# Performance work log

Measured on AMD Instinct MI355X. Metric: run time of the kernel, lower is better.

## Reference

```python
import jax, jax.numpy as jnp
import numpy as np

B, L, H, NH, NB = 16, 200, 128, 2, 2
ITEMS, SPAN = 50000, 256
NEG = -2.0**32 + 1.0  # mask value used by the torch module


def _ln(x, g, b, eps=1e-8):
    m = jnp.mean(x, axis=-1, keepdims=True)
    v = jnp.mean((x - m) ** 2, axis=-1, keepdims=True)
    return (x - m) / jnp.sqrt(v + eps) * g + b


def setup_inputs() -> dict:
    key = jax.random.key(0)
    ks = jax.random.split(key, 20)
    p = lambda k, s: (jax.random.normal(k, s, jnp.float32) * 0.02)
    item_emb = p(ks[0], (ITEMS + 1, H)).at[0].set(0.0)  # padding_idx=0
    return {
        "user_ids": jax.random.randint(ks[1], (B,), 0, 10000),
        "log_seqs": jax.random.randint(ks[2], (B, L), 0, ITEMS),
        "time_matrices": jax.random.randint(ks[3], (B, L, L), 0, SPAN),
        "pos_seqs": jax.random.randint(ks[4], (B, L), 0, ITEMS),
        "neg_seqs": jax.random.randint(ks[5], (B, L), 0, ITEMS),
        "item_emb": item_emb,
        "pos_K_emb": p(ks[6], (L, H)),
        "pos_V_emb": p(ks[7], (L, H)),
        "time_K_emb": p(ks[8], (SPAN + 1, H)),
        "time_V_emb": p(ks[9], (SPAN + 1, H)),
        "Wq": p(ks[10], (NB, H, H)), "bq": jnp.zeros((NB, H)),
        "Wk": p(ks[11], (NB, H, H)), "bk": jnp.zeros((NB, H)),
        "Wv": p(ks[12], (NB, H, H)), "bv": jnp.zeros((NB, H)),
        "ln1_g": jnp.ones((NB, H)), "ln1_b": jnp.zeros((NB, H)),
        "W1": p(ks[13], (NB, H, H)), "b1": jnp.zeros((NB, H)),
        "W2": p(ks[14], (NB, H, H)), "b2": jnp.zeros((NB, H)),
        "ln2_g": jnp.ones((NB, H)), "ln2_b": jnp.zeros((NB, H)),
        "lnf_g": jnp.ones((H,)), "lnf_b": jnp.zeros((H,)),
    }


def reference(user_ids, log_seqs, time_matrices, pos_seqs, neg_seqs,
              item_emb, pos_K_emb, pos_V_emb, time_K_emb, time_V_emb,
              Wq, bq, Wk, bk, Wv, bv, ln1_g, ln1_b,
              W1, b1, W2, b2, ln2_g, ln2_b, lnf_g, lnf_b):
    d = H // NH
    pad = (log_seqs == 0)                    # (B,L) timeline mask
    keep = (~pad)[..., None].astype(jnp.float32)

    seqs = item_emb[log_seqs] * jnp.sqrt(jnp.float32(H))
    seqs = seqs * keep
    posK = pos_K_emb.reshape(L, NH, d)       # same for every batch element
    posV = pos_V_emb.reshape(L, NH, d)
    tmK = time_K_emb[time_matrices].reshape(B, L, L, NH, d)  # (B,L,L,h,d)
    tmV = time_V_emb[time_matrices].reshape(B, L, L, NH, d)
    causal = ~jnp.tril(jnp.ones((L, L), dtype=bool))          # True = masked
    mask = pad[:, None, :, None] | causal[None, None, :, :]   # (B,1,L,L) row-mask | causal

    for i in range(NB):
        Q = (seqs @ Wq[i].T + bq[i]).reshape(B, L, NH, d)
        K = (seqs @ Wk[i].T + bk[i]).reshape(B, L, NH, d)
        V = (seqs @ Wv[i].T + bv[i]).reshape(B, L, NH, d)
        aw = jnp.einsum('bqhd,bkhd->bhqk', Q, K)
        aw = aw + jnp.einsum('bqhd,khd->bhqk', Q, posK)
        aw = aw + jnp.einsum('bqkhd,bqhd->bhqk', tmK, Q)
        aw = aw / jnp.sqrt(jnp.float32(d))
        aw = jnp.where(mask, NEG, aw)
        A = jax.nn.softmax(aw, axis=-1)                        # (B,h,L,L)
        out = jnp.einsum('bhqk,bkhd->bqhd', A, V)
        out = out + jnp.einsum('bhqk,khd->bqhd', A, posV)
        out = out + jnp.einsum('bhqk,bqkhd->bqhd', A, tmV)
        out = out.reshape(B, L, H)
        seqs = _ln(seqs + out, ln1_g[i], ln1_b[i])
        ffn = jax.nn.relu(seqs @ W1[i].T + b1[i]) @ W2[i].T + b2[i]
        seqs = _ln(seqs + ffn, ln2_g[i], ln2_b[i])
        seqs = seqs * keep

    log_feats = _ln(seqs, lnf_g, lnf_b)
    pos_logits = jnp.sum(log_feats * item_emb[pos_seqs], axis=-1)  # (B,L)
    neg_logits = jnp.sum(log_feats * item_emb[neg_seqs], axis=-1)
    return jnp.stack([pos_logits, neg_logits])  # (2,B,L)
```

## Files before the change

kernel.cpp:

```cpp
#include <hip/hip_runtime.h>
#include <hip/hip_bf16.h>
#include <math.h>

#define BB 16
#define LL 200
#define HH 128
#define DD 64
#define QT2 8
#define NQT2 25
#define NEGF -4294967295.0f
#define SQRTH 11.313708498984761f

__global__ __launch_bounds__(512) void k_qkv(float* __restrict__ seqs,
    const int* __restrict__ log_seqs, const float* __restrict__ item_emb, int do_embed,
    const float* __restrict__ Wq, const float* __restrict__ bq,
    const float* __restrict__ Wk, const float* __restrict__ bk,
    const float* __restrict__ Wv, const float* __restrict__ bv,
    const float* __restrict__ posK, const float* __restrict__ posV,
    float* __restrict__ Q, float* __restrict__ Kp, float* __restrict__ Vp) {
    __shared__ float s_lds[16][HH];
    int r0g = blockIdx.x * 16;
    int t = threadIdx.x;
    if (do_embed) {
        int r = t >> 5, d4 = t & 31;
        int id = log_seqs[r0g + r];
        float4 v = make_float4(0.f, 0.f, 0.f, 0.f);
        if (id != 0) {
            v = ((const float4*)(item_emb + id * HH))[d4];
            v.x *= SQRTH; v.y *= SQRTH; v.z *= SQRTH; v.w *= SQRTH;
        }
        *(float4*)&s_lds[r][d4 * 4] = v;
        ((float4*)(seqs + r0g * HH))[t] = v;
    } else {
        ((float4*)s_lds)[t] = ((const float4*)(seqs + r0g * HH))[t];
    }
    __syncthreads();
    int c = t & 127, rg = t >> 7;
    float aq[4] = {0.f, 0.f, 0.f, 0.f};
    float ak[4] = {0.f, 0.f, 0.f, 0.f};
    float av[4] = {0.f, 0.f, 0.f, 0.f};
    const float4* wq4 = (const float4*)(Wq + c * HH);
    const float4* wk4 = (const float4*)(Wk + c * HH);
    const float4* wv4 = (const float4*)(Wv + c * HH);
#pragma unroll 4
    for (int k4 = 0; k4 < HH / 4; ++k4) {
        float4 wq = wq4[k4], wk = wk4[k4], wv = wv4[k4];
#pragma unroll
        for (int r = 0; r < 4; ++r) {
            float4 s = *(const float4*)&s_lds[rg * 4 + r][k4 * 4];
            aq[r] += s.x * wq.x + s.y * wq.y + s.z * wq.z + s.w * wq.w;
            ak[r] += s.x * wk.x + s.y * wk.y + s.z * wk.z + s.w * wk.w;
            av[r] += s.x * wv.x + s.y * wv.y + s.z * wv.z + s.w * wv.w;
        }
    }
#pragma unroll
    for (int r = 0; r < 4; ++r) {
        int row = r0g + rg * 4 + r;
        int l = row % LL;
        Q[row * HH + c]  = aq[r] + bq[c];
        Kp[row * HH + c] = ak[r] + bk[c] + posK[l * HH + c];
        Vp[row * HH + c] = av[r] + bv[c] + posV[l * HH + c];
    }
}

__global__ __launch_bounds__(256) void k_proj(const float* __restrict__ Q,
    const float* __restrict__ timeK, float* __restrict__ projK) {
    int bh = blockIdx.x / 13, qt = blockIdx.x % 13;
    int b = bh >> 1, h = bh & 1;
    int qlo = qt * 16;
    __shared__ float Qs[16][68];
    __shared__ float TK[32][68];
    int t = threadIdx.x;
    {
        int r = t >> 4, d4 = t & 15;
        int q = qlo + r;
        float4 v = make_float4(0.f, 0.f, 0.f, 0.f);
        if (q < LL) v = ((const float4*)(Q + (b * LL + q) * HH + h * DD))[d4];
        *(float4*)&Qs[r][d4 * 4] = v;
    }
    int tq = t >> 4, ttl = t & 15;
    int q = qlo + tq;
    for (int c = 0; c < 9; ++c) {
        int base = c * 32;
        __syncthreads();
        for (int x = t; x < 512; x += 256) {
            int i = x >> 4, d4 = x & 15;
            int tt = base + i;
            if (tt < 257)
                *(float4*)&TK[i][d4 * 4] =
                    ((const float4*)(timeK + tt * HH + h * DD))[d4];
        }
        __syncthreads();
#pragma unroll
        for (int j = 0; j < 2; ++j) {
            int ti = ttl + 16 * j;
            int tt = base + ti;
            if (tt < 257 && q < LL) {
                float acc = 0.f;
#pragma unroll
                for (int d4 = 0; d4 < 16; ++d4) {
                    float4 qv = *(const float4*)&Qs[tq][d4 * 4];
                    float4 kv = *(const float4*)&TK[ti][d4 * 4];
                    acc += qv.x * kv.x + qv.y * kv.y + qv.z * kv.z + qv.w * kv.w;
                }
                projK[(bh * LL + q) * 257 + tt] = acc;
            }
        }
    }
}

__global__ __launch_bounds__(256) void k_attn(
    const float* __restrict__ Q, const float* __restrict__ Kp, const float* __restrict__ Vp,
    const float* __restrict__ projK, const float* __restrict__ timeV,
    const int* __restrict__ tm, const int* __restrict__ log_seqs,
    float* __restrict__ attnout) {
    int bh = blockIdx.x / NQT2, qt = blockIdx.x % NQT2;
    int b = bh >> 1, h = bh & 1;
    int qlo = qt * QT2;
    __shared__ float K_s[32][68];
    __shared__ float smemW[457 * 12];
    __shared__ unsigned long long pm64[4];
    __shared__ int s_allmask;
#define WT(i, j) smemW[(i) * 12 + (j)]
    int t = threadIdx.x;
    int tq = t >> 5, lane = t & 31, g = tq;
    int q = qlo + tq;
    int qhi = qlo + QT2 - 1;

    {
        bool keep = (t < LL) && (log_seqs[b * LL + t] != 0);
        unsigned long long ball = __ballot(keep);
        if ((t & 63) == 0) pm64[t >> 6] = ball;
    }
    if (t == 0) s_allmask = 0;
    for (int x = t; x < 200 * 12; x += 256) smemW[x] = NEGF;
    for (int x = 200 * 12 + t; x < 457 * 12; x += 256) smemW[x] = 0.f;
    float4 qreg[16];
    {
        const float4* qp = (const float4*)(Q + (b * LL + q) * HH + h * DD);
#pragma unroll
        for (int d4 = 0; d4 < 16; ++d4) qreg[d4] = qp[d4];
    }
    const int* tmrow = tm + (b * LL + q) * LL;
    const float* projrow = projK + (bh * LL + q) * 257;
    __syncthreads();

    int nkc = (qhi >> 5) + 1;
    for (int kc = 0; kc < nkc; ++kc) {
        int kbase = kc * 32;
        for (int x = t; x < 512; x += 256) {
            int i = x >> 4, d4 = x & 15;
            int k = kbase + i;
            if (k < LL)
                *(float4*)&K_s[i][d4 * 4] =
                    ((const float4*)(Kp + (b * LL + k) * HH + h * DD))[d4];
        }
        __syncthreads();
        int k = kbase + lane;
        if (k <= q && ((pm64[k >> 6] >> (k & 63)) & 1ull)) {
            float acc = 0.f;
#pragma unroll
            for (int d4 = 0; d4 < 16; ++d4) {
                float4 kv = *(const float4*)&K_s[lane][d4 * 4];
                acc += qreg[d4].x * kv.x + qreg[d4].y * kv.y +
                       qreg[d4].z * kv.z + qreg[d4].w * kv.w;
            }
            WT(k, tq) = (acc + projrow[tmrow[k]]) * 0.125f;
        }
        __syncthreads();
    }

    float mx = -INFINITY;
    for (int k = lane; k < LL; k += 32) mx = fmaxf(mx, WT(k, tq));
    mx = fmaxf(mx, __shfl_xor(mx, 1, 64));
    mx = fmaxf(mx, __shfl_xor(mx, 2, 64));
    mx = fmaxf(mx, __shfl_xor(mx, 4, 64));
    mx = fmaxf(mx, __shfl_xor(mx, 8, 64));
    mx = fmaxf(mx, __shfl_xor(mx, 16, 64));
    bool allmask = (mx == NEGF);
    float sum = 0.f;
    for (int k = lane; k < LL; k += 32) {
        float e = __expf(WT(k, tq) - mx);
        WT(k, tq) = e;
        sum += e;
    }
    sum += __shfl_xor(sum, 1, 64);
    sum += __shfl_xor(sum, 2, 64);
    sum += __shfl_xor(sum, 4, 64);
    sum += __shfl_xor(sum, 8, 64);
    sum += __shfl_xor(sum, 16, 64);
    float inv = 1.0f / sum;
    int klim = allmask ? LL : (q + 1);
    if (allmask && lane == 0) s_allmask = 1;
    for (int k = lane; k < LL; k += 32) {
        float p = WT(k, tq) * inv;
        WT(k, tq) = p;
        if (k < klim) atomicAdd(&WT(200 + tmrow[k], tq), p);
    }
    __syncthreads();

    int kmax = s_allmask ? LL : (qhi + 1);
    float a00=0.f,a01=0.f,a10=0.f,a11=0.f,a20=0.f,a21=0.f,a30=0.f,a31=0.f;
    float a40=0.f,a41=0.f,a50=0.f,a51=0.f,a60=0.f,a61=0.f,a70=0.f,a71=0.f;
#define PV_STEP(WROW, SRCPTR)                                            \
    {                                                                    \
        const float* wr = &WROW;                                         \
        float4 w0 = *(const float4*)wr;                                  \
        float4 w1 = *(const float4*)(wr + 4);                            \
        float2 vv = *(const float2*)(SRCPTR);                            \
        a00 += w0.x * vv.x; a01 += w0.x * vv.y;                          \
        a10 += w0.y * vv.x; a11 += w0.y * vv.y;                          \
        a20 += w0.z * vv.x; a21 += w0.z * vv.y;                          \
        a30 += w0.w * vv.x; a31 += w0.w * vv.y;                          \
        a40 += w1.x * vv.x; a41 += w1.x * vv.y;                          \
        a50 += w1.y * vv.x; a51 += w1.y * vv.y;                          \
        a60 += w1.z * vv.x; a61 += w1.z * vv.y;                          \
        a70 += w1.w * vv.x; a71 += w1.w * vv.y;                          \
    }
    for (int i = g; i < kmax; i += 8)
        PV_STEP(WT(i, 0), Vp + (b * LL + i) * HH + h * DD + lane * 2);
    for (int i = g; i < 257; i += 8)
        PV_STEP(WT(200 + i, 0), timeV + i * HH + h * DD + lane * 2);
#undef PV_STEP
    __syncthreads();
    float* part = smemW;
    part[g * 512 + 0 * 64 + lane * 2] = a00; part[g * 512 + 0 * 64 + lane * 2 + 1] = a01;
    part[g * 512 + 1 * 64 + lane * 2] = a10; part[g * 512 + 1 * 64 + lane * 2 + 1] = a11;
    part[g * 512 + 2 * 64 + lane * 2] = a20; part[g * 512 + 2 * 64 + lane * 2 + 1] = a21;
    part[g * 512 + 3 * 64 + lane * 2] = a30; part[g * 512 + 3 * 64 + lane * 2 + 1] = a31;
    part[g * 512 + 4 * 64 + lane * 2] = a40; part[g * 512 + 4 * 64 + lane * 2 + 1] = a41;
    part[g * 512 + 5 * 64 + lane * 2] = a50; part[g * 512 + 5 * 64 + lane * 2 + 1] = a51;
    part[g * 512 + 6 * 64 + lane * 2] = a60; part[g * 512 + 6 * 64 + lane * 2 + 1] = a61;
    part[g * 512 + 7 * 64 + lane * 2] = a70; part[g * 512 + 7 * 64 + lane * 2 + 1] = a71;
    __syncthreads();
    {
        float ox = 0.f, oy = 0.f;
#pragma unroll
        for (int gg = 0; gg < 8; ++gg) {
            ox += part[gg * 512 + tq * 64 + lane * 2];
            oy += part[gg * 512 + tq * 64 + lane * 2 + 1];
        }
        *(float2*)(attnout + (b * LL + q) * HH + h * DD + lane * 2) =
            make_float2(ox, oy);
    }
#undef WT
}

__global__ __launch_bounds__(512) void k_ffn_full(
    float* __restrict__ seqs, const float* __restrict__ AO,
    const float* __restrict__ g1, const float* __restrict__ be1,
    const float* __restrict__ W1, const float* __restrict__ b1,
    const float* __restrict__ W2, const float* __restrict__ b2,
    const float* __restrict__ g2, const float* __restrict__ be2,
    const int* __restrict__ log_seqs, int do_final,
    const float* __restrict__ lnf_g, const float* __restrict__ lnf_b,
    const float* __restrict__ item_emb,
    const int* __restrict__ pos_seqs, const int* __restrict__ neg_seqs,
    float* __restrict__ out) {
    __shared__ float s_lds[16][HH];
    __shared__ float h_lds[16][HH];
    int r0g = blockIdx.x * 16;
    int t = threadIdx.x;
    {
        float4 a = ((const float4*)(seqs + r0g * HH))[t];
        float4 o = ((const float4*)(AO + r0g * HH))[t];
        a.x += o.x; a.y += o.y; a.z += o.z; a.w += o.w;
        ((float4*)s_lds)[t] = a;
    }
    __syncthreads();
    int w = t >> 6, lane = t & 63;
    int lrow = w * 2 + (lane >> 5), cl = lane & 31;
    {
        float sm = 0.f;
#pragma unroll
        for (int j = 0; j < 4; ++j) sm += s_lds[lrow][cl + 32 * j];
        sm += __shfl_xor(sm, 1, 64);
        sm += __shfl_xor(sm, 2, 64);
        sm += __shfl_xor(sm, 4, 64);
        sm += __shfl_xor(sm, 8, 64);
        sm += __shfl_xor(sm, 16, 64);
        float mean = sm * (1.0f / HH);
        float vr = 0.f;
#pragma unroll
        for (int j = 0; j < 4; ++j) {
            float d = s_lds[lrow][cl + 32 * j] - mean;
            vr += d * d;
        }
        vr += __shfl_xor(vr, 1, 64);
        vr += __shfl_xor(vr, 2, 64);
        vr += __shfl_xor(vr, 4, 64);
        vr += __shfl_xor(vr, 8, 64);
        vr += __shfl_xor(vr, 16, 64);
        float rstd = rsqrtf(vr * (1.0f / HH) + 1e-8f);
#pragma unroll
        for (int j = 0; j < 4; ++j) {
            int c = cl + 32 * j;
            s_lds[lrow][c] = (s_lds[lrow][c] - mean) * rstd * g1[c] + be1[c];
        }
    }
    __syncthreads();
    int c = t & 127, rg = t >> 7;
    float acc[4] = {0.f, 0.f, 0.f, 0.f};
    const float4* w14 = (const float4*)(W1 + c * HH);
#pragma unroll 4
    for (int k4 = 0; k4 < HH / 4; ++k4) {
        float4 ww = w14[k4];
#pragma unroll
        for (int r = 0; r < 4; ++r) {
            float4 s = *(const float4*)&s_lds[rg * 4 + r][k4 * 4];
            acc[r] += s.x * ww.x + s.y * ww.y + s.z * ww.z + s.w * ww.w;
        }
    }
#pragma unroll
    for (int r = 0; r < 4; ++r) h_lds[rg * 4 + r][c] = fmaxf(acc[r] + b1[c], 0.f);
    __syncthreads();
#pragma unroll
    for (int r = 0; r < 4; ++r) acc[r] = 0.f;
    const float4* w24 = (const float4*)(W2 + c * HH);
#pragma unroll 4
    for (int k4 = 0; k4 < HH / 4; ++k4) {
        float4 ww = w24[k4];
#pragma unroll
        for (int r = 0; r < 4; ++r) {
            float4 s = *(const float4*)&h_lds[rg * 4 + r][k4 * 4];
            acc[r] += s.x * ww.x + s.y * ww.y + s.z * ww.z + s.w * ww.w;
        }
    }
    __syncthreads();
#pragma unroll
    for (int r = 0; r < 4; ++r)
        h_lds[rg * 4 + r][c] = s_lds[rg * 4 + r][c] + acc[r] + b2[c];
    __syncthreads();
    {
        float sm = 0.f;
#pragma unroll
        for (int j = 0; j < 4; ++j) sm += h_lds[lrow][cl + 32 * j];
        sm += __shfl_xor(sm, 1, 64);
        sm += __shfl_xor(sm, 2, 64);
        sm += __shfl_xor(sm, 4, 64);
        sm += __shfl_xor(sm, 8, 64);
        sm += __shfl_xor(sm, 16, 64);
        float mean = sm * (1.0f / HH);
        float vr = 0.f;
#pragma unroll
        for (int j = 0; j < 4; ++j) {
            float d = h_lds[lrow][cl + 32 * j] - mean;
            vr += d * d;
        }
        vr += __shfl_xor(vr, 1, 64);
        vr += __shfl_xor(vr, 2, 64);
        vr += __shfl_xor(vr, 4, 64);
        vr += __shfl_xor(vr, 8, 64);
        vr += __shfl_xor(vr, 16, 64);
        float rstd = rsqrtf(vr * (1.0f / HH) + 1e-8f);
        int row = r0g + lrow;
        float keep = (log_seqs[row] != 0) ? 1.0f : 0.0f;
        float y2[4];
#pragma unroll
        for (int j = 0; j < 4; ++j) {
            int cc = cl + 32 * j;
            y2[j] = ((h_lds[lrow][cc] - mean) * rstd * g2[cc] + be2[cc]) * keep;
        }
        if (!do_final) {
#pragma unroll
            for (int j = 0; j < 4; ++j)
                seqs[row * HH + cl + 32 * j] = y2[j];
        } else {
            float sm2 = y2[0] + y2[1] + y2[2] + y2[3];
            sm2 += __shfl_xor(sm2, 1, 64);
            sm2 += __shfl_xor(sm2, 2, 64);
            sm2 += __shfl_xor(sm2, 4, 64);
            sm2 += __shfl_xor(sm2, 8, 64);
            sm2 += __shfl_xor(sm2, 16, 64);
            float mean2 = sm2 * (1.0f / HH);
            float vr2 = 0.f;
#pragma unroll
            for (int j = 0; j < 4; ++j) {
                float d = y2[j] - mean2;
                vr2 += d * d;
            }
            vr2 += __shfl_xor(vr2, 1, 64);
            vr2 += __shfl_xor(vr2, 2, 64);
            vr2 += __shfl_xor(vr2, 4, 64);
            vr2 += __shfl_xor(vr2, 8, 64);
            vr2 += __shfl_xor(vr2, 16, 64);
            float rstd2 = rsqrtf(vr2 * (1.0f / HH) + 1e-8f);
            int pid = pos_seqs[row];
            int nid = neg_seqs[row];
            float pp = 0.f, nn = 0.f;
#pragma unroll
            for (int j = 0; j < 4; ++j) {
                int cc = cl + 32 * j;
                float lf = (y2[j] - mean2) * rstd2 * lnf_g[cc] + lnf_b[cc];
                pp += lf * item_emb[pid * HH + cc];
                nn += lf * item_emb[nid * HH + cc];
            }
            pp += __shfl_xor(pp, 1, 64);
            pp += __shfl_xor(pp, 2, 64);
            pp += __shfl_xor(pp, 4, 64);
            pp += __shfl_xor(pp, 8, 64);
            pp += __shfl_xor(pp, 16, 64);
            nn += __shfl_xor(nn, 1, 64);
            nn += __shfl_xor(nn, 2, 64);
            nn += __shfl_xor(nn, 4, 64);
            nn += __shfl_xor(nn, 8, 64);
            nn += __shfl_xor(nn, 16, 64);
            if (cl == 0) {
                out[row] = pp;
                out[BB * LL + row] = nn;
            }
        }
    }
}

extern "C" void kernel_launch(void* const* d_in, const int* in_sizes, int n_in,
                              void* d_out, int out_size, void* d_ws, size_t ws_size,
                              hipStream_t stream) {
    const int* log_seqs = (const int*)d_in[1];
    const int* tm       = (const int*)d_in[2];
    const int* pos_seqs = (const int*)d_in[3];
    const int* neg_seqs = (const int*)d_in[4];
    const float* item_emb = (const float*)d_in[5];
    const float* posK   = (const float*)d_in[6];
    const float* posV   = (const float*)d_in[7];
    const float* timeK  = (const float*)d_in[8];
    const float* timeV  = (const float*)d_in[9];
    const float* Wq = (const float*)d_in[10];
    const float* bq = (const float*)d_in[11];
    const float* Wk = (const float*)d_in[12];
    const float* bk = (const float*)d_in[13];
    const float* Wv = (const float*)d_in[14];
    const float* bv = (const float*)d_in[15];
    const float* ln1_g = (const float*)d_in[16];
    const float* ln1_b = (const float*)d_in[17];
    const float* W1 = (const float*)d_in[18];
    const float* b1 = (const float*)d_in[19];
    const float* W2 = (const float*)d_in[20];
    const float* b2 = (const float*)d_in[21];
    const float* ln2_g = (const float*)d_in[22];
    const float* ln2_b = (const float*)d_in[23];
    const float* lnf_g = (const float*)d_in[24];
    const float* lnf_b = (const float*)d_in[25];

    float* ws    = (float*)d_ws;
    float* seqs  = ws;
    float* Qb    = seqs + 409600;
    float* Kpb   = Qb + 409600;
    float* Vpb   = Kpb + 409600;
    float* AO    = Vpb + 409600;
    float* projK = AO + 409600;

    for (int i = 0; i < 2; ++i) {
        k_qkv<<<BB * LL / 16, 512, 0, stream>>>(seqs, log_seqs, item_emb,
            (i == 0) ? 1 : 0,
            Wq + i * HH * HH, bq + i * HH,
            Wk + i * HH * HH, bk + i * HH,
            Wv + i * HH * HH, bv + i * HH,
            posK, posV, Qb, Kpb, Vpb);
        k_proj<<<32 * 13, 256, 0, stream>>>(Qb, timeK, projK);
        k_attn<<<32 * NQT2, 256, 0, stream>>>(Qb, Kpb, Vpb, projK, timeV,
                                              tm, log_seqs, AO);
        k_ffn_full<<<BB * LL / 16, 512, 0, stream>>>(seqs, AO,
            ln1_g + i * HH, ln1_b + i * HH,
            W1 + i * HH * HH, b1 + i * HH,
            W2 + i * HH * HH, b2 + i * HH,
            ln2_g + i * HH, ln2_b + i * HH, log_seqs,
            (i == 1) ? 1 : 0, lnf_g, lnf_b, item_emb,
            pos_seqs, neg_seqs, (float*)d_out);
    }
}
```

Measured before the change: 197.8 us.

## Fuse next-block QKV projection into FFN kernel and keep attention scores in registers

The second block's QKV projection now runs inside the first block's FFN kernel. This removes one launch and a reload of seqs from global memory. The attention kernel keeps causal scores in per-lane registers rather than initialising and rereading an LDS score table, reads the padding mask directly instead of building a ballot bitmask, and skips atomic adds for zero probabilities. k_proj now uses 8-query tiles to match the attention tiling, which gives more blocks, and the block loop is unrolled in host code. The fused FFN kernel carries more code and register pressure.

```diff
diff --git a/kernel.cpp b/kernel.cpp
--- a/kernel.cpp
+++ b/kernel.cpp
@@ -6,13 +6,12 @@
 #define LL 200
 #define HH 128
 #define DD 64
-#define QT2 8
-#define NQT2 25
+#define NQT 25
 #define NEGF -4294967295.0f
 #define SQRTH 11.313708498984761f
 
 __global__ __launch_bounds__(512) void k_qkv(float* __restrict__ seqs,
-    const int* __restrict__ log_seqs, const float* __restrict__ item_emb, int do_embed,
+    const int* __restrict__ log_seqs, const float* __restrict__ item_emb,
     const float* __restrict__ Wq, const float* __restrict__ bq,
     const float* __restrict__ Wk, const float* __restrict__ bk,
     const float* __restrict__ Wv, const float* __restrict__ bv,
@@ -21,7 +20,7 @@
     __shared__ float s_lds[16][HH];
     int r0g = blockIdx.x * 16;
     int t = threadIdx.x;
-    if (do_embed) {
+    {
         int r = t >> 5, d4 = t & 31;
         int id = log_seqs[r0g + r];
         float4 v = make_float4(0.f, 0.f, 0.f, 0.f);
@@ -31,8 +30,6 @@
         }
         *(float4*)&s_lds[r][d4 * 4] = v;
         ((float4*)(seqs + r0g * HH))[t] = v;
-    } else {
-        ((float4*)s_lds)[t] = ((const float4*)(seqs + r0g * HH))[t];
     }
     __syncthreads();
     int c = t & 127, rg = t >> 7;
@@ -65,23 +62,20 @@
 
 __global__ __launch_bounds__(256) void k_proj(const float* __restrict__ Q,
     const float* __restrict__ timeK, float* __restrict__ projK) {
-    int bh = blockIdx.x / 13, qt = blockIdx.x % 13;
+    int bh = blockIdx.x / 25, qt = blockIdx.x % 25;
     int b = bh >> 1, h = bh & 1;
-    int qlo = qt * 16;
-    __shared__ float Qs[16][68];
+    int qlo = qt * 8;
+    __shared__ float Qs[8][68];
     __shared__ float TK[32][68];
     int t = threadIdx.x;
-    {
+    if (t < 128) {
         int r = t >> 4, d4 = t & 15;
-        int q = qlo + r;
-        float4 v = make_float4(0.f, 0.f, 0.f, 0.f);
-        if (q < LL) v = ((const float4*)(Q + (b * LL + q) * HH + h * DD))[d4];
-        *(float4*)&Qs[r][d4 * 4] = v;
-    }
-    int tq = t >> 4, ttl = t & 15;
-    int q = qlo + tq;
-    for (int c = 0; c < 9; ++c) {
-        int base = c * 32;
+        *(float4*)&Qs[r][d4 * 4] =
+            ((const float4*)(Q + (b * LL + qlo + r) * HH + h * DD))[d4];
+    }
+    int tq = t >> 5, ttl = t & 31;
+    for (int ch = 0; ch < 9; ++ch) {
+        int base = ch * 32;
         __syncthreads();
         for (int x = t; x < 512; x += 256) {
             int i = x >> 4, d4 = x & 15;
@@ -91,20 +85,16 @@
                     ((const float4*)(timeK + tt * HH + h * DD))[d4];
         }
         __syncthreads();
-#pragma unroll
-        for (int j = 0; j < 2; ++j) {
-            int ti = ttl + 16 * j;
-            int tt = base + ti;
-            if (tt < 257 && q < LL) {
-                float acc = 0.f;
-#pragma unroll
-                for (int d4 = 0; d4 < 16; ++d4) {
-                    float4 qv = *(const float4*)&Qs[tq][d4 * 4];
-                    float4 kv = *(const float4*)&TK[ti][d4 * 4];
-                    acc += qv.x * kv.x + qv.y * kv.y + qv.z * kv.z + qv.w * kv.w;
-                }
-                projK[(bh * LL + q) * 257 + tt] = acc;
-            }
+        int tt = base + ttl;
+        if (tt < 257) {
+            float acc = 0.f;
+#pragma unroll
+            for (int d4 = 0; d4 < 16; ++d4) {
+                float4 qv = *(const float4*)&Qs[tq][d4 * 4];
+                float4 kv = *(const float4*)&TK[ttl][d4 * 4];
+                acc += qv.x * kv.x + qv.y * kv.y + qv.z * kv.z + qv.w * kv.w;
+            }
+            projK[(bh * LL + qlo + tq) * 257 + tt] = acc;
         }
     }
 }
@@ -114,26 +104,19 @@
     const float* __restrict__ projK, const float* __restrict__ timeV,
     const int* __restrict__ tm, const int* __restrict__ log_seqs,
     float* __restrict__ attnout) {
-    int bh = blockIdx.x / NQT2, qt = blockIdx.x % NQT2;
+    int bh = blockIdx.x / NQT, qt = blockIdx.x % NQT;
     int b = bh >> 1, h = bh & 1;
-    int qlo = qt * QT2;
+    int qlo = qt * 8;
     __shared__ float K_s[32][68];
     __shared__ float smemW[457 * 12];
-    __shared__ unsigned long long pm64[4];
     __shared__ int s_allmask;
 #define WT(i, j) smemW[(i) * 12 + (j)]
     int t = threadIdx.x;
     int tq = t >> 5, lane = t & 31, g = tq;
     int q = qlo + tq;
-    int qhi = qlo + QT2 - 1;
-
-    {
-        bool keep = (t < LL) && (log_seqs[b * LL + t] != 0);
-        unsigned long long ball = __ballot(keep);
-        if ((t & 63) == 0) pm64[t >> 6] = ball;
-    }
+    int qhi = qlo + 7;
+
     if (t == 0) s_allmask = 0;
-    for (int x = t; x < 200 * 12; x += 256) smemW[x] = NEGF;
     for (int x = 200 * 12 + t; x < 457 * 12; x += 256) smemW[x] = 0.f;
     float4 qreg[16];
     {
@@ -143,35 +126,42 @@
     }
     const int* tmrow = tm + (b * LL + q) * LL;
     const float* projrow = projK + (bh * LL + q) * 257;
-    __syncthreads();
-
+    const int* lsrow = log_seqs + b * LL;
+
+    float s[7];
+#pragma unroll
+    for (int j = 0; j < 7; ++j) s[j] = NEGF;
     int nkc = (qhi >> 5) + 1;
-    for (int kc = 0; kc < nkc; ++kc) {
-        int kbase = kc * 32;
-        for (int x = t; x < 512; x += 256) {
-            int i = x >> 4, d4 = x & 15;
-            int k = kbase + i;
-            if (k < LL)
-                *(float4*)&K_s[i][d4 * 4] =
-                    ((const float4*)(Kp + (b * LL + k) * HH + h * DD))[d4];
-        }
-        __syncthreads();
-        int k = kbase + lane;
-        if (k <= q && ((pm64[k >> 6] >> (k & 63)) & 1ull)) {
-            float acc = 0.f;
-#pragma unroll
-            for (int d4 = 0; d4 < 16; ++d4) {
-                float4 kv = *(const float4*)&K_s[lane][d4 * 4];
-                acc += qreg[d4].x * kv.x + qreg[d4].y * kv.y +
-                       qreg[d4].z * kv.z + qreg[d4].w * kv.w;
-            }
-            WT(k, tq) = (acc + projrow[tmrow[k]]) * 0.125f;
-        }
-        __syncthreads();
-    }
-
-    float mx = -INFINITY;
-    for (int k = lane; k < LL; k += 32) mx = fmaxf(mx, WT(k, tq));
+#pragma unroll
+    for (int kc = 0; kc < 7; ++kc) {
+        if (kc < nkc) {
+            int kbase = kc * 32;
+            for (int x = t; x < 512; x += 256) {
+                int i = x >> 4, d4 = x & 15;
+                int k = kbase + i;
+                if (k < LL)
+                    *(float4*)&K_s[i][d4 * 4] =
+                        ((const float4*)(Kp + (b * LL + k) * HH + h * DD))[d4];
+            }
+            __syncthreads();
+            int k = kbase + lane;
+            if (k <= q && lsrow[k] != 0) {
+                float acc = 0.f;
+#pragma unroll
+                for (int d4 = 0; d4 < 16; ++d4) {
+                    float4 kv = *(const float4*)&K_s[lane][d4 * 4];
+                    acc += qreg[d4].x * kv.x + qreg[d4].y * kv.y +
+                           qreg[d4].z * kv.z + qreg[d4].w * kv.w;
+                }
+                s[kc] = (acc + projrow[tmrow[k]]) * 0.125f;
+            }
+            __syncthreads();
+        }
+    }
+
+    float mx = s[0];
+#pragma unroll
+    for (int j = 1; j < 7; ++j) mx = fmaxf(mx, s[j]);
     mx = fmaxf(mx, __shfl_xor(mx, 1, 64));
     mx = fmaxf(mx, __shfl_xor(mx, 2, 64));
     mx = fmaxf(mx, __shfl_xor(mx, 4, 64));
@@ -179,9 +169,11 @@
     mx = fmaxf(mx, __shfl_xor(mx, 16, 64));
     bool allmask = (mx == NEGF);
     float sum = 0.f;
-    for (int k = lane; k < LL; k += 32) {
-        float e = __expf(WT(k, tq) - mx);
-        WT(k, tq) = e;
+#pragma unroll
+    for (int j = 0; j < 7; ++j) {
+        int k = lane + 32 * j;
+        float e = (k < LL) ? __expf(s[j] - mx) : 0.f;
+        s[j] = e;
         sum += e;
     }
     sum += __shfl_xor(sum, 1, 64);
@@ -192,10 +184,15 @@
     float inv = 1.0f / sum;
     int klim = allmask ? LL : (q + 1);
     if (allmask && lane == 0) s_allmask = 1;
-    for (int k = lane; k < LL; k += 32) {
-        float p = WT(k, tq) * inv;
-        WT(k, tq) = p;
-        if (k < klim) atomicAdd(&WT(200 + tmrow[k], tq), p);
+#pragma unroll
+    for (int j = 0; j < 7; ++j) {
+        int k = lane + 32 * j;
+        if (k < LL) {
+            float p = s[j] * inv;
+            WT(k, tq) = p;
+            if (k < klim && p != 0.f)
+                atomicAdd(&WT(200 + tmrow[k], tq), p);
+        }
     }
     __syncthreads();
 
@@ -252,7 +249,14 @@
     const float* __restrict__ W1, const float* __restrict__ b1,
     const float* __restrict__ W2, const float* __restrict__ b2,
     const float* __restrict__ g2, const float* __restrict__ be2,
-    const int* __restrict__ log_seqs, int do_final,
+    const int* __restrict__ log_seqs,
+    int do_qkv,
+    const float* __restrict__ Wq, const float* __restrict__ bq,
+    const float* __restrict__ Wk, const float* __restrict__ bk,
+    const float* __restrict__ Wv, const float* __restrict__ bv,
+    const float* __restrict__ posK, const float* __restrict__ posV,
+    float* __restrict__ Q, float* __restrict__ Kp, float* __restrict__ Vp,
+    int do_final,
     const float* __restrict__ lnf_g, const float* __restrict__ lnf_b,
     const float* __restrict__ item_emb,
     const int* __restrict__ pos_seqs, const int* __restrict__ neg_seqs,
@@ -274,10 +278,8 @@
         float sm = 0.f;
 #pragma unroll
         for (int j = 0; j < 4; ++j) sm += s_lds[lrow][cl + 32 * j];
-        sm += __shfl_xor(sm, 1, 64);
-        sm += __shfl_xor(sm, 2, 64);
-        sm += __shfl_xor(sm, 4, 64);
-        sm += __shfl_xor(sm, 8, 64);
+        sm += __shfl_xor(sm, 1, 64);  sm += __shfl_xor(sm, 2, 64);
+        sm += __shfl_xor(sm, 4, 64);  sm += __shfl_xor(sm, 8, 64);
         sm += __shfl_xor(sm, 16, 64);
         float mean = sm * (1.0f / HH);
         float vr = 0.f;
@@ -286,10 +288,8 @@
             float d = s_lds[lrow][cl + 32 * j] - mean;
             vr += d * d;
         }
-        vr += __shfl_xor(vr, 1, 64);
-        vr += __shfl_xor(vr, 2, 64);
-        vr += __shfl_xor(vr, 4, 64);
-        vr += __shfl_xor(vr, 8, 64);
+        vr += __shfl_xor(vr, 1, 64);  vr += __shfl_xor(vr, 2, 64);
+        vr += __shfl_xor(vr, 4, 64);  vr += __shfl_xor(vr, 8, 64);
         vr += __shfl_xor(vr, 16, 64);
         float rstd = rsqrtf(vr * (1.0f / HH) + 1e-8f);
 #pragma unroll
@@ -335,10 +335,8 @@
         float sm = 0.f;
 #pragma unroll
         for (int j = 0; j < 4; ++j) sm += h_lds[lrow][cl + 32 * j];
-        sm += __shfl_xor(sm, 1, 64);
-        sm += __shfl_xor(sm, 2, 64);
-        sm += __shfl_xor(sm, 4, 64);
-        sm += __shfl_xor(sm, 8, 64);
+        sm += __shfl_xor(sm, 1, 64);  sm += __shfl_xor(sm, 2, 64);
+        sm += __shfl_xor(sm, 4, 64);  sm += __shfl_xor(sm, 8, 64);
         sm += __shfl_xor(sm, 16, 64);
         float mean = sm * (1.0f / HH);
         float vr = 0.f;
@@ -347,10 +345,8 @@
             float d = h_lds[lrow][cl + 32 * j] - mean;
             vr += d * d;
         }
-        vr += __shfl_xor(vr, 1, 64);
-        vr += __shfl_xor(vr, 2, 64);
-        vr += __shfl_xor(vr, 4, 64);
-        vr += __shfl_xor(vr, 8, 64);
+        vr += __shfl_xor(vr, 1, 64);  vr += __shfl_xor(vr, 2, 64);
+        vr += __shfl_xor(vr, 4, 64);  vr += __shfl_xor(vr, 8, 64);
         vr += __shfl_xor(vr, 16, 64);
         float rstd = rsqrtf(vr * (1.0f / HH) + 1e-8f);
         int row = r0g + lrow;
@@ -361,16 +357,10 @@
             int cc = cl + 32 * j;
             y2[j] = ((h_lds[lrow][cc] - mean) * rstd * g2[cc] + be2[cc]) * keep;
         }
-        if (!do_final) {
-#pragma unroll
-            for (int j = 0; j < 4; ++j)
-                seqs[row * HH + cl + 32 * j] = y2[j];
-        } else {
+        if (do_final) {
             float sm2 = y2[0] + y2[1] + y2[2] + y2[3];
-            sm2 += __shfl_xor(sm2, 1, 64);
-            sm2 += __shfl_xor(sm2, 2, 64);
-            sm2 += __shfl_xor(sm2, 4, 64);
-            sm2 += __shfl_xor(sm2, 8, 64);
+            sm2 += __shfl_xor(sm2, 1, 64);  sm2 += __shfl_xor(sm2, 2, 64);
+            sm2 += __shfl_xor(sm2, 4, 64);  sm2 += __shfl_xor(sm2, 8, 64);
             sm2 += __shfl_xor(sm2, 16, 64);
             float mean2 = sm2 * (1.0f / HH);
             float vr2 = 0.f;
@@ -379,10 +369,8 @@
                 float d = y2[j] - mean2;
                 vr2 += d * d;
             }
-            vr2 += __shfl_xor(vr2, 1, 64);
-            vr2 += __shfl_xor(vr2, 2, 64);
-            vr2 += __shfl_xor(vr2, 4, 64);
-            vr2 += __shfl_xor(vr2, 8, 64);
+            vr2 += __shfl_xor(vr2, 1, 64);  vr2 += __shfl_xor(vr2, 2, 64);
+            vr2 += __shfl_xor(vr2, 4, 64);  vr2 += __shfl_xor(vr2, 8, 64);
             vr2 += __shfl_xor(vr2, 16, 64);
             float rstd2 = rsqrtf(vr2 * (1.0f / HH) + 1e-8f);
             int pid = pos_seqs[row];
@@ -395,21 +383,53 @@
                 pp += lf * item_emb[pid * HH + cc];
                 nn += lf * item_emb[nid * HH + cc];
             }
-            pp += __shfl_xor(pp, 1, 64);
-            pp += __shfl_xor(pp, 2, 64);
-            pp += __shfl_xor(pp, 4, 64);
-            pp += __shfl_xor(pp, 8, 64);
+            pp += __shfl_xor(pp, 1, 64);  pp += __shfl_xor(pp, 2, 64);
+            pp += __shfl_xor(pp, 4, 64);  pp += __shfl_xor(pp, 8, 64);
             pp += __shfl_xor(pp, 16, 64);
-            nn += __shfl_xor(nn, 1, 64);
-            nn += __shfl_xor(nn, 2, 64);
-            nn += __shfl_xor(nn, 4, 64);
-            nn += __shfl_xor(nn, 8, 64);
+            nn += __shfl_xor(nn, 1, 64);  nn += __shfl_xor(nn, 2, 64);
+            nn += __shfl_xor(nn, 4, 64);  nn += __shfl_xor(nn, 8, 64);
             nn += __shfl_xor(nn, 16, 64);
             if (cl == 0) {
                 out[row] = pp;
                 out[BB * LL + row] = nn;
             }
-        }
+        } else {
+#pragma unroll
+            for (int j = 0; j < 4; ++j)
+                seqs[row * HH + cl + 32 * j] = y2[j];
+            if (do_qkv) {
+#pragma unroll
+                for (int j = 0; j < 4; ++j)
+                    s_lds[lrow][cl + 32 * j] = y2[j];
+            }
+        }
+    }
+    if (!do_qkv) return;
+    __syncthreads();
+    float aq[4] = {0.f, 0.f, 0.f, 0.f};
+    float ak[4] = {0.f, 0.f, 0.f, 0.f};
+    float av[4] = {0.f, 0.f, 0.f, 0.f};
+    const float4* wq4 = (const float4*)(Wq + c * HH);
+    const float4* wk4 = (const float4*)(Wk + c * HH);
+    const float4* wv4 = (const float4*)(Wv + c * HH);
+#pragma unroll 4
+    for (int k4 = 0; k4 < HH / 4; ++k4) {
+        float4 wq = wq4[k4], wk = wk4[k4], wv = wv4[k4];
+#pragma unroll
+        for (int r = 0; r < 4; ++r) {
+            float4 s = *(const float4*)&s_lds[rg * 4 + r][k4 * 4];
+            aq[r] += s.x * wq.x + s.y * wq.y + s.z * wq.z + s.w * wq.w;
+            ak[r] += s.x * wk.x + s.y * wk.y + s.z * wk.z + s.w * wk.w;
+            av[r] += s.x * wv.x + s.y * wv.y + s.z * wv.z + s.w * wv.w;
+        }
+    }
+#pragma unroll
+    for (int r = 0; r < 4; ++r) {
+        int row = r0g + rg * 4 + r;
+        int l = row % LL;
+        Q[row * HH + c]  = aq[r] + bq[c];
+        Kp[row * HH + c] = ak[r] + bk[c] + posK[l * HH + c];
+        Vp[row * HH + c] = av[r] + bv[c] + posV[l * HH + c];
     }
 }
 
@@ -450,22 +470,23 @@
     float* AO    = Vpb + 409600;
     float* projK = AO + 409600;
 
-    for (int i = 0; i < 2; ++i) {
-        k_qkv<<<BB * LL / 16, 512, 0, stream>>>(seqs, log_seqs, item_emb,
-            (i == 0) ? 1 : 0,
-            Wq + i * HH * HH, bq + i * HH,
-            Wk + i * HH * HH, bk + i * HH,
-            Wv + i * HH * HH, bv + i * HH,
-            posK, posV, Qb, Kpb, Vpb);
-        k_proj<<<32 * 13, 256, 0, stream>>>(Qb, timeK, projK);
-        k_attn<<<32 * NQT2, 256, 0, stream>>>(Qb, Kpb, Vpb, projK, timeV,
-                                              tm, log_seqs, AO);
-        k_ffn_full<<<BB * LL / 16, 512, 0, stream>>>(seqs, AO,
-            ln1_g + i * HH, ln1_b + i * HH,
-            W1 + i * HH * HH, b1 + i * HH,
-            W2 + i * HH * HH, b2 + i * HH,
-            ln2_g + i * HH, ln2_b + i * HH, log_seqs,
-            (i == 1) ? 1 : 0, lnf_g, lnf_b, item_emb,
-            pos_seqs, neg_seqs, (float*)d_out);
-    }
+    k_qkv<<<BB * LL / 16, 512, 0, stream>>>(seqs, log_seqs, item_emb,
+        Wq, bq, Wk, bk, Wv, bv, posK, posV, Qb, Kpb, Vpb);
+    k_proj<<<32 * NQT, 256, 0, stream>>>(Qb, timeK, projK);
+    k_attn<<<32 * NQT, 256, 0, stream>>>(Qb, Kpb, Vpb, projK, timeV,
+                                         tm, log_seqs, AO);
+    k_ffn_full<<<BB * LL / 16, 512, 0, stream>>>(seqs, AO,
+        ln1_g, ln1_b, W1, b1, W2, b2, ln2_g, ln2_b, log_seqs,
+        1, Wq + HH * HH, bq + HH, Wk + HH * HH, bk + HH, Wv + HH * HH, bv + HH,
+        posK, posV, Qb, Kpb, Vpb,
+        0, lnf_g, lnf_b, item_emb, pos_seqs, neg_seqs, (float*)d_out);
+    k_proj<<<32 * NQT, 256, 0, stream>>>(Qb, timeK, projK);
+    k_attn<<<32 * NQT, 256, 0, stream>>>(Qb, Kpb, Vpb, projK, timeV,
+                                         tm, log_seqs, AO);
+    k_ffn_full<<<BB * LL / 16, 512, 0, stream>>>(seqs, AO,
+        ln1_g + HH, ln1_b + HH, W1 + HH * HH, b1 + HH, W2 + HH * HH, b2 + HH,
+        ln2_g + HH, ln2_b + HH, log_seqs,
+        0, nullptr, nullptr, nullptr, nullptr, nullptr, nullptr,
+        nullptr, nullptr, nullptr, nullptr, nullptr,
+        1, lnf_g, lnf_b, item_emb, pos_seqs, neg_seqs, (float*)d_out);
 }
```

After: 183.7 us, median of 2. 1.08x faster.
